# Performance work log

Measured on AMD Instinct MI355X. Metric: run time of the kernel, lower is better.

## Reference

```python
import jax, jax.numpy as jnp
import numpy as np

N_HEADS = 16


def setup_inputs() -> dict:
    key = jax.random.key(0)
    ks = jax.random.split(key, 5)
    E = 1024
    x = jax.random.normal(ks[0], (2, 2048, E), dtype=jnp.float32)
    s = 1.0 / np.sqrt(E)
    Wq = jax.random.normal(ks[1], (E, E), dtype=jnp.float32) * s
    Wk = jax.random.normal(ks[2], (E, E), dtype=jnp.float32) * s
    Wv = jax.random.normal(ks[3], (E, E), dtype=jnp.float32) * s
    Wo = jax.random.normal(ks[4], (E, E), dtype=jnp.float32) * s
    bo = jnp.zeros((E,), dtype=jnp.float32)
    return {"x": x, "Wq": Wq, "Wk": Wk, "Wv": Wv, "Wo": Wo, "bo": bo}


def reference(x, Wq, Wk, Wv, Wo, bo):
    B, S, E = x.shape
    H = N_HEADS
    D = E // H
    # project and split heads: [B, H, S, D]
    def split_heads(y):
        return y.reshape(B, S, H, D).transpose(0, 2, 1, 3)
    q = split_heads(x @ Wq)
    k = split_heads(x @ Wk)
    v = split_heads(x @ Wv)
    # full score matrix [B, H, S, S]
    scores = jnp.einsum('bhqd,bhkd->bhqk', q, k)
    causal = jnp.triu(jnp.ones((S, S), dtype=bool), k=1)
    scores = jnp.where(causal, -jnp.inf, scores)
    attn = jax.nn.softmax(scores / jnp.sqrt(jnp.float32(D)), axis=-1)
    # dropout rate is 0.0 -> identity
    ctx = jnp.einsum('bhqk,bhkd->bhqd', attn, v)
    ctx = ctx.transpose(0, 2, 1, 3).reshape(B, S, E)
    return ctx @ Wo + bo
```

## Files before the change

kernel.cpp:

```cpp
#include <hip/hip_runtime.h>
#include <stdint.h>


#define N_HEADS 16
#define HD 64
#define SEQ 2048
#define EMB 1024

typedef __attribute__((ext_vector_type(8))) short s16x8;
typedef __attribute__((ext_vector_type(4))) float f32x4;
typedef __attribute__((ext_vector_type(16))) float f32x16;

#define QSCALE 0.18033688f

template <bool B> struct BC { static constexpr bool value = B; };

__device__ __forceinline__ short f2b(float f) {
  union { float f; uint32_t u; } v; v.f = f;
  uint32_t u = v.u;
  u += 0x7fffu + ((u >> 16) & 1u);
  return (short)(u >> 16);
}

__device__ __forceinline__ uint32_t pk2(float a, float b) {
  union { float f; uint32_t u; } x, y; x.f = a; y.f = b;
  return ((x.u + 0x8000u) >> 16) | ((y.u + 0x8000u) & 0xffff0000u);
}

__device__ __forceinline__ float exp2a(float x) {
  float r; asm("v_exp_f32 %0, %1" : "=v"(r) : "v"(x)); return r;
}

__device__ __forceinline__ void gll16(const void* g, void* l) {
  __builtin_amdgcn_global_load_lds((const __attribute__((address_space(1))) void*)g,
                                   (__attribute__((address_space(3))) void*)l, 16, 0, 0);
}

#define SWZ(row, chunk) ((((row) * 8) + ((chunk) ^ ((row) & 7))) * 8)

__global__ __launch_bounds__(256) void k_prep(const float* __restrict__ x,
                                              const float* __restrict__ W0,
                                              const float* __restrict__ W1,
                                              const float* __restrict__ W2,
                                              const float* __restrict__ W3,
                                              short* __restrict__ xb,
                                              short* __restrict__ wt) {
  const int z = blockIdx.x, t = threadIdx.x;
  if (z < 4096) {
    int i = z * 256 + t;
    float4 v = ((const float4*)x)[i];
    short4 o;
    o.x = f2b(v.x); o.y = f2b(v.y); o.z = f2b(v.z); o.w = f2b(v.w);
    ((short4*)xb)[i] = o;
  } else {
    __shared__ float tile[32][33];
    int bz = z - 4096;
    int w = bz >> 10, rem = bz & 1023;
    int bn = (rem & 31) * 32, bk = (rem >> 5) * 32;
    const float* W = w == 0 ? W0 : w == 1 ? W1 : w == 2 ? W2 : W3;
    short* o = wt + (size_t)w * EMB * EMB;
    int tx = t & 31, ty = t >> 5;
    for (int i = ty; i < 32; i += 8)
      tile[i][tx] = W[(size_t)(bk + i) * EMB + bn + tx];
    __syncthreads();
    for (int i = ty; i < 32; i += 8)
      o[(size_t)(bn + i) * EMB + bk + tx] = f2b(tile[tx][i]);
  }
}

template <int MODE>
__global__ __launch_bounds__(256) void k_gemm(const short* __restrict__ A,
                                              const short* __restrict__ BT,
                                              void* __restrict__ outp,
                                              const float* __restrict__ bias) {
  constexpr int MAIN = 4 * 4096;
  constexpr int EPIL = (MODE == 1) ? 0 : 128 * 132;
  constexpr int SMSZ = MAIN > EPIL ? MAIN : EPIL;
  __shared__ alignas(16) short smem[SMSZ];

  const int t = threadIdx.x;
  const int by = blockIdx.y;
  const int m0 = blockIdx.x * 128;
  const short* Bp = BT + (size_t)by * (128 * EMB);
  const int wave = t >> 6, lane = t & 63;
  const int wm = (wave >> 1) * 64, wn = (wave & 1) * 64;
  const int l31 = lane & 31, lh = lane >> 5;

  const int srow = lane >> 2;
  const int soff = ((lane & 3) ^ (srow & 3)) * 8;

  auto stage = [&](int kb, int p) {
    short* as = smem + p * 4096;
    short* bs = smem + 8192 + p * 4096;
#pragma unroll
    for (int i = 0; i < 2; i++) {
      int rb = wave * 32 + i * 16;
      gll16(A + (size_t)(m0 + rb + srow) * EMB + kb + soff, &as[rb * 32]);
      gll16(Bp + (size_t)(rb + srow) * EMB + kb + soff, &bs[rb * 32]);
    }
  };
  auto frd = [&](const short* sb, int row, int kh) -> s16x8 {
    int c = kh * 2 + lh;
    return *(const s16x8*)&sb[row * 32 + ((c ^ (row & 3)) * 8)];
  };

  f32x16 acc[2][2] = {};

  auto kloop = [&](auto SWC) {
    constexpr bool SW = decltype(SWC)::value;
    int pb = 0;
    stage(0, 0);
    for (int kb = 0; kb < EMB; kb += 32) {
      __syncthreads();
      if (kb + 32 < EMB) stage(kb + 32, pb ^ 1);
      const short* as = smem + pb * 4096;
      const short* bs = smem + 8192 + pb * 4096;
      s16x8 af[2][2], bf[2][2];
#pragma unroll
      for (int mt = 0; mt < 2; mt++)
#pragma unroll
        for (int kh = 0; kh < 2; kh++) af[mt][kh] = frd(as, wm + mt * 32 + l31, kh);
#pragma unroll
      for (int nt = 0; nt < 2; nt++)
#pragma unroll
        for (int kh = 0; kh < 2; kh++) bf[nt][kh] = frd(bs, wn + nt * 32 + l31, kh);
#pragma unroll
      for (int mt = 0; mt < 2; mt++)
#pragma unroll
        for (int nt = 0; nt < 2; nt++)
#pragma unroll
          for (int kh = 0; kh < 2; kh++)
            acc[mt][nt] = SW
              ? __builtin_amdgcn_mfma_f32_32x32x16_bf16(bf[nt][kh], af[mt][kh], acc[mt][nt], 0, 0, 0)
              : __builtin_amdgcn_mfma_f32_32x32x16_bf16(af[mt][kh], bf[nt][kh], acc[mt][nt], 0, 0, 0);
      pb ^= 1;
    }
  };

  if (MODE == 1 || by < 16) kloop(BC<true>{});
  else                      kloop(BC<false>{});

  if (MODE == 0) {
    if (by < 16) {
      __syncthreads();
      short* Vls = smem;
      const int wsel = by >> 3;
      const float qs = (wsel == 0) ? QSCALE : 1.0f;
      const int n0l = (by & 7) * 128;
#pragma unroll
      for (int mt = 0; mt < 2; mt++) {
        int mr = wm + mt * 32 + l31;
#pragma unroll
        for (int nt = 0; nt < 2; nt++)
#pragma unroll
          for (int g = 0; g < 4; g++) {
            uint2 w;
            w.x = pk2(acc[mt][nt][4 * g + 0] * qs, acc[mt][nt][4 * g + 1] * qs);
            w.y = pk2(acc[mt][nt][4 * g + 2] * qs, acc[mt][nt][4 * g + 3] * qs);
            *(uint2*)&Vls[mr * 132 + wn + nt * 32 + g * 8 + 4 * lh] = w;
          }
      }
      __syncthreads();
      short* ob = (short*)outp + (size_t)wsel * (4u * 1024 * 1024);
      const int bb = m0 >> 11, ss0 = m0 & (SEQ - 1);
#pragma unroll
      for (int i = 0; i < 8; i++) {
        int mrow = i * 16 + (t >> 4);
        int ncol = (t & 15) * 8;
        int e = n0l + ncol, hh = e >> 6, dd = e & 63;
        *(uint4*)&ob[(((size_t)(bb * N_HEADS + hh) * SEQ) + ss0 + mrow) * 64 + dd] =
            *(const uint4*)&Vls[mrow * 132 + ncol];
      }
    } else {
      __syncthreads();
      short* Vls = smem;
#pragma unroll
      for (int nt = 0; nt < 2; nt++) {
        int nl = wn + nt * 32 + l31;
#pragma unroll
        for (int mt = 0; mt < 2; mt++)
#pragma unroll
          for (int g = 0; g < 4; g++) {
            uint2 w;
            w.x = pk2(acc[mt][nt][4 * g + 0], acc[mt][nt][4 * g + 1]);
            w.y = pk2(acc[mt][nt][4 * g + 2], acc[mt][nt][4 * g + 3]);
            *(uint2*)&Vls[nl * 132 + wm + mt * 32 + g * 8 + 4 * lh] = w;
          }
      }
      __syncthreads();
      short* obv = (short*)outp + (size_t)8 * 1024 * 1024;
      const int n0l = (by & 7) * 128;
      const int bb = m0 >> 11, ss0 = m0 & (SEQ - 1);
#pragma unroll
      for (int i = 0; i < 8; i++) {
        int nl = i * 16 + (t >> 4);
        int mc = (t & 15) * 8;
        int e = n0l + nl, hh = e >> 6, dd = e & 63;
        *(uint4*)&obv[((size_t)((bb * N_HEADS + hh) * HD + dd)) * SEQ + ss0 + mc] =
            *(const uint4*)&Vls[nl * 132 + mc];
      }
    }
  } else {
    float* of = (float*)outp;
    const int n0 = by * 128;
#pragma unroll
    for (int mt = 0; mt < 2; mt++) {
      int mg = m0 + wm + mt * 32 + l31;
#pragma unroll
      for (int nt = 0; nt < 2; nt++)
#pragma unroll
        for (int g = 0; g < 4; g++) {
          int ng = n0 + wn + nt * 32 + g * 8 + 4 * lh;
          f32x4 bv = *(const f32x4*)&bias[ng];
          f32x4 w;
          w[0] = acc[mt][nt][4 * g + 0] + bv[0];
          w[1] = acc[mt][nt][4 * g + 1] + bv[1];
          w[2] = acc[mt][nt][4 * g + 2] + bv[2];
          w[3] = acc[mt][nt][4 * g + 3] + bv[3];
          *(f32x4*)&of[(size_t)mg * EMB + ng] = w;
        }
    }
  }
}

__global__ __launch_bounds__(512) void k_attn(const short* __restrict__ Q,
                                              const short* __restrict__ K,
                                              const short* __restrict__ Vt,
                                              short* __restrict__ ctx) {
  __shared__ alignas(16) short UQP[128 * 72];
  __shared__ alignas(16) short Ks0[64 * 64], Ks1[64 * 64];
  __shared__ alignas(16) short Vs0[64 * 64], Vs1[64 * 64];

  const int t = threadIdx.x, wave = t >> 6, lane = t & 63;
  const int ml = lane & 15, quad = lane >> 4;
  const int bh = blockIdx.x;
  const int qb = 15 - (int)blockIdx.y;
  const size_t base = (size_t)bh * SEQ * HD;
  const int q0 = qb * 128, wq = q0 + wave * 16;

  const int sr = lane >> 3;
  const int sc = ((lane & 7) ^ sr) * 8;

#pragma unroll
  for (int i = 0; i < 2; i++) {
    int r8 = wave * 16 + i * 8;
    gll16(Q + base + (size_t)(q0 + r8 + sr) * HD + sc, &UQP[r8 * 64]);
  }
  auto stageKV = [&](int kt, short* kd, short* vd) {
    const int kbase = kt * 64;
    const int r8 = wave * 8;
    gll16(K + base + (size_t)(kbase + r8 + sr) * HD + sc, &kd[r8 * 64]);
    gll16(Vt + base + (size_t)(r8 + sr) * SEQ + kbase + sc, &vd[r8 * 64]);
  };

  f32x4 cacc[4] = {};
  float li = 0.f;
  short* Pw = &UQP[wave * 16 * 72];

  stageKV(0, Ks0, Vs0);
  __syncthreads();

  s16x8 qf[2];
#pragma unroll
  for (int c = 0; c < 2; c++)
    qf[c] = *(const s16x8*)&UQP[SWZ(wave * 16 + ml, 4 * c + quad)];
  __syncthreads();

  auto tile_body = [&](int kt, const short* kd, const short* vd) {
    const int kbase = kt * 64;
    if (kbase > wq + 15) return;
    const bool diag = (kbase + 63 > wq);
    f32x4 st[4];
#pragma unroll
    for (int nt = 0; nt < 4; nt++) {
      int row = nt * 16 + ml;
      s16x8 kf0 = *(const s16x8*)&kd[SWZ(row, quad)];
      s16x8 kf1 = *(const s16x8*)&kd[SWZ(row, 4 + quad)];
      f32x4 z = {};
      z = __builtin_amdgcn_mfma_f32_16x16x32_bf16(kf0, qf[0], z, 0, 0, 0);
      st[nt] = __builtin_amdgcn_mfma_f32_16x16x32_bf16(kf1, qf[1], z, 0, 0, 0);
    }
    const int qg = wq + ml;
    float rsum = 0.f;
#pragma unroll
    for (int nt = 0; nt < 4; nt++) {
      float p0 = exp2a(st[nt][0]);
      float p1 = exp2a(st[nt][1]);
      float p2 = exp2a(st[nt][2]);
      float p3 = exp2a(st[nt][3]);
      if (diag) {
        int kk = kbase + nt * 16 + quad * 4;
        if (kk + 0 > qg) p0 = 0.f;
        if (kk + 1 > qg) p1 = 0.f;
        if (kk + 2 > qg) p2 = 0.f;
        if (kk + 3 > qg) p3 = 0.f;
      }
      rsum += (p0 + p1) + (p2 + p3);
      uint2 w; w.x = pk2(p0, p1); w.y = pk2(p2, p3);
      *(uint2*)&Pw[ml * 72 + nt * 16 + quad * 4] = w;
    }
    li += rsum;
    __builtin_amdgcn_wave_barrier();

    s16x8 pf[2];
#pragma unroll
    for (int c = 0; c < 2; c++)
      pf[c] = *(const s16x8*)&Pw[ml * 72 + c * 32 + quad * 8];
#pragma unroll
    for (int mt = 0; mt < 4; mt++) {
      int row = mt * 16 + ml;
      s16x8 vf0 = *(const s16x8*)&vd[SWZ(row, quad)];
      s16x8 vf1 = *(const s16x8*)&vd[SWZ(row, 4 + quad)];
      cacc[mt] = __builtin_amdgcn_mfma_f32_16x16x32_bf16(vf0, pf[0], cacc[mt], 0, 0, 0);
      cacc[mt] = __builtin_amdgcn_mfma_f32_16x16x32_bf16(vf1, pf[1], cacc[mt], 0, 0, 0);
    }
  };

  const int nkt = 2 * qb + 2;
  for (int kt = 0; kt < nkt; kt += 2) {
    stageKV(kt + 1, Ks1, Vs1);
    tile_body(kt, Ks0, Vs0);
    __syncthreads();
    if (kt + 2 < nkt) stageKV(kt + 2, Ks0, Vs0);
    tile_body(kt + 1, Ks1, Vs1);
    __syncthreads();
  }

  li += __shfl_xor(li, 16, 64);
  li += __shfl_xor(li, 32, 64);
  float inv = 1.0f / li;
#pragma unroll
  for (int mt = 0; mt < 4; mt++) {
    uint2 w;
    w.x = pk2(cacc[mt][0] * inv, cacc[mt][1] * inv);
    w.y = pk2(cacc[mt][2] * inv, cacc[mt][3] * inv);
    *(uint2*)&Pw[ml * 72 + mt * 16 + quad * 4] = w;
  }
  __builtin_amdgcn_wave_barrier();
  const int b = bh >> 4, h = bh & 15;
#pragma unroll
  for (int i = 0; i < 2; i++) {
    int row = i * 8 + (lane >> 3);
    int q = wq + row;
    size_t gbase = ((size_t)(b * SEQ + q)) * EMB + h * 64 + (lane & 7) * 8;
    *(uint4*)&ctx[gbase] = *(const uint4*)&Pw[row * 72 + (lane & 7) * 8];
  }
}

extern "C" void kernel_launch(void* const* d_in, const int* in_sizes, int n_in,
                              void* d_out, int out_size, void* d_ws, size_t ws_size,
                              hipStream_t stream) {
  const float* x  = (const float*)d_in[0];
  const float* Wq = (const float*)d_in[1];
  const float* Wk = (const float*)d_in[2];
  const float* Wv = (const float*)d_in[3];
  const float* Wo = (const float*)d_in[4];
  const float* bo = (const float*)d_in[5];
  float* out = (float*)d_out;

  short* ws = (short*)d_ws;
  short* xb  = ws;
  short* wt  = ws + (size_t)4 * 1024 * 1024;
  short* qkv = ws + (size_t)8 * 1024 * 1024;

  k_prep<<<8192, 256, 0, stream>>>(x, Wq, Wk, Wv, Wo, xb, wt);
  k_gemm<0><<<dim3(32, 24), 256, 0, stream>>>(xb, wt, qkv, nullptr);
  k_attn<<<dim3(32, 16), 512, 0, stream>>>(qkv, qkv + (size_t)4 * 1024 * 1024,
                                           qkv + (size_t)8 * 1024 * 1024, xb);
  k_gemm<1><<<dim3(32, 8), 256, 0, stream>>>(xb, wt + (size_t)3 * 1024 * 1024, out, bo);
}
```

Before: 172.3 us.

## Add dedicated 256x256-tile QKV GEMM kernel with 4-stage async LDS pipeline

Replaces the 128x128-tile QKV projection GEMM with a new 512-thread kernel using 256x256 tiles and 16x16x32 bf16 MFMAs. It adds a 4-buffer global-to-LDS load pipeline with explicit vmcnt waits and raised wave priority around the MFMA bursts. The epilogue writes through LDS in two halves for the head-split Q/K and transposed V layouts, and k_gemm is reduced to the output-projection path only. The aim is more operand reuse per loaded byte and better overlap of loads with math. The trade-off is a grid of only 192 blocks, fewer than the CU count, and 128KB of LDS per block.

```diff
diff --git a/kernel.cpp b/kernel.cpp
--- a/kernel.cpp
+++ b/kernel.cpp
@@ -68,15 +68,149 @@
   }
 }
 
+__global__ __launch_bounds__(512, 2) void k_qkv(const short* __restrict__ A,
+                                                const short* __restrict__ BT,
+                                                short* __restrict__ qkv) {
+  __shared__ alignas(16) short smem[65536];
+  const int t = threadIdx.x;
+  const int bx = blockIdx.x, by = blockIdx.y;
+  const int m0 = bx * 256;
+  const short* Bp = BT + (size_t)by * (256 * EMB);
+  const int wave = t >> 6, lane = t & 63;
+  const int ml = lane & 15, quad = lane >> 4;
+  const int wm = (wave >> 2) * 128, wn = (wave & 3) * 64;
+  const int wsel = by >> 2;
+
+  auto stage = [&](int kt) {
+    short* sa = smem + (kt & 3) * 16384;
+    short* sb = sa + 8192;
+    const int k0 = kt * 32;
+#pragma unroll
+    for (int j = 0; j < 2; j++) {
+      int ci = j * 512 + t;
+      int r = ci >> 2;
+      int col = ((ci & 3) ^ (r & 3)) * 8;
+      size_t ldso = (size_t)(j * 512 + (t & ~63)) * 8;
+      gll16(A + (size_t)(m0 + r) * EMB + k0 + col, sa + ldso);
+      gll16(Bp + (size_t)r * EMB + k0 + col, sb + ldso);
+    }
+  };
+
+  f32x4 acc[8][4] = {};
+
+  stage(0); stage(1); stage(2);
+
+  auto kloop = [&](auto SWC) {
+    constexpr bool SW = decltype(SWC)::value;
+    for (int T = 0; T < 32; T++) {
+      const short* sa = smem + (T & 3) * 16384;
+      const short* sb = sa + 8192;
+      if (T < 30) asm volatile("s_waitcnt vmcnt(8)" ::: "memory");
+      else        asm volatile("s_waitcnt vmcnt(0)" ::: "memory");
+      __builtin_amdgcn_s_barrier();
+      __builtin_amdgcn_sched_barrier(0);
+      if (T + 3 < 32) stage(T + 3);
+      s16x8 af[8];
+#pragma unroll
+      for (int mt = 0; mt < 8; mt++) {
+        int row = wm + mt * 16 + ml;
+        af[mt] = *(const s16x8*)&sa[row * 32 + ((quad ^ (row & 3)) * 8)];
+      }
+#pragma unroll
+      for (int n2 = 0; n2 < 2; n2++) {
+        int r0 = wn + (n2 * 2 + 0) * 16 + ml;
+        int r1 = wn + (n2 * 2 + 1) * 16 + ml;
+        s16x8 b0 = *(const s16x8*)&sb[r0 * 32 + ((quad ^ (r0 & 3)) * 8)];
+        s16x8 b1 = *(const s16x8*)&sb[r1 * 32 + ((quad ^ (r1 & 3)) * 8)];
+        __builtin_amdgcn_s_setprio(1);
+#pragma unroll
+        for (int mt = 0; mt < 8; mt++) {
+          if (SW) {
+            acc[mt][n2 * 2 + 0] = __builtin_amdgcn_mfma_f32_16x16x32_bf16(b0, af[mt], acc[mt][n2 * 2 + 0], 0, 0, 0);
+            acc[mt][n2 * 2 + 1] = __builtin_amdgcn_mfma_f32_16x16x32_bf16(b1, af[mt], acc[mt][n2 * 2 + 1], 0, 0, 0);
+          } else {
+            acc[mt][n2 * 2 + 0] = __builtin_amdgcn_mfma_f32_16x16x32_bf16(af[mt], b0, acc[mt][n2 * 2 + 0], 0, 0, 0);
+            acc[mt][n2 * 2 + 1] = __builtin_amdgcn_mfma_f32_16x16x32_bf16(af[mt], b1, acc[mt][n2 * 2 + 1], 0, 0, 0);
+          }
+        }
+        __builtin_amdgcn_s_setprio(0);
+      }
+    }
+  };
+
+  if (wsel < 2) kloop(BC<true>{});
+  else          kloop(BC<false>{});
+
+  __syncthreads();
+
+  const int b = m0 >> 11, s0 = m0 & (SEQ - 1);
+  const int n0in = (by & 3) * 256;
+  if (wsel < 2) {
+    short* ob = qkv + (size_t)wsel * (4u * 1024 * 1024);
+    const float qs = (wsel == 0) ? QSCALE : 1.0f;
+#pragma unroll
+    for (int half = 0; half < 2; half++) {
+      if ((wm >> 7) == half) {
+#pragma unroll
+        for (int mt = 0; mt < 8; mt++) {
+          int lr = mt * 16 + ml;
+#pragma unroll
+          for (int nt = 0; nt < 4; nt++) {
+            uint2 w;
+            w.x = pk2(acc[mt][nt][0] * qs, acc[mt][nt][1] * qs);
+            w.y = pk2(acc[mt][nt][2] * qs, acc[mt][nt][3] * qs);
+            *(uint2*)&smem[lr * 264 + wn + nt * 16 + quad * 4] = w;
+          }
+        }
+      }
+      __syncthreads();
+#pragma unroll
+      for (int p = 0; p < 8; p++) {
+        int r = p * 16 + (t >> 5), c = t & 31;
+        int e = n0in + c * 8, hh = e >> 6, dd = e & 63;
+        *(uint4*)&ob[(((size_t)(b * N_HEADS + hh) * SEQ) + s0 + half * 128 + r) * 64 + dd] =
+            *(const uint4*)&smem[r * 264 + c * 8];
+      }
+      __syncthreads();
+    }
+  } else {
+    short* obv = qkv + (size_t)8 * 1024 * 1024;
+#pragma unroll
+    for (int half = 0; half < 2; half++) {
+      if ((wm >> 7) == half) {
+#pragma unroll
+        for (int mt = 0; mt < 8; mt++) {
+          int lr = mt * 16 + quad * 4;
+#pragma unroll
+          for (int nt = 0; nt < 4; nt++) {
+            int colL = wn + nt * 16 + ml;
+            uint2 w;
+            w.x = pk2(acc[mt][nt][0], acc[mt][nt][1]);
+            w.y = pk2(acc[mt][nt][2], acc[mt][nt][3]);
+            *(uint2*)&smem[colL * 136 + lr] = w;
+          }
+        }
+      }
+      __syncthreads();
+#pragma unroll
+      for (int p = 0; p < 8; p++) {
+        int colL = p * 32 + (t >> 4);
+        int sc = (t & 15) * 8;
+        int e = n0in + colL, hh = e >> 6, dd = e & 63;
+        *(uint4*)&obv[((size_t)(b * N_HEADS + hh) * HD + dd) * SEQ + s0 + half * 128 + sc] =
+            *(const uint4*)&smem[colL * 136 + sc];
+      }
+      __syncthreads();
+    }
+  }
+}
+
 template <int MODE>
 __global__ __launch_bounds__(256) void k_gemm(const short* __restrict__ A,
                                               const short* __restrict__ BT,
                                               void* __restrict__ outp,
                                               const float* __restrict__ bias) {
-  constexpr int MAIN = 4 * 4096;
-  constexpr int EPIL = (MODE == 1) ? 0 : 128 * 132;
-  constexpr int SMSZ = MAIN > EPIL ? MAIN : EPIL;
-  __shared__ alignas(16) short smem[SMSZ];
+  __shared__ alignas(16) short smem[4 * 4096];
 
   const int t = threadIdx.x;
   const int by = blockIdx.y;
@@ -106,8 +240,7 @@
 
   f32x16 acc[2][2] = {};
 
-  auto kloop = [&](auto SWC) {
-    constexpr bool SW = decltype(SWC)::value;
+  {
     int pb = 0;
     stage(0, 0);
     for (int kb = 0; kb < EMB; kb += 32) {
@@ -130,77 +263,12 @@
         for (int nt = 0; nt < 2; nt++)
 #pragma unroll
           for (int kh = 0; kh < 2; kh++)
-            acc[mt][nt] = SW
-              ? __builtin_amdgcn_mfma_f32_32x32x16_bf16(bf[nt][kh], af[mt][kh], acc[mt][nt], 0, 0, 0)
-              : __builtin_amdgcn_mfma_f32_32x32x16_bf16(af[mt][kh], bf[nt][kh], acc[mt][nt], 0, 0, 0);
+            acc[mt][nt] = __builtin_amdgcn_mfma_f32_32x32x16_bf16(bf[nt][kh], af[mt][kh], acc[mt][nt], 0, 0, 0);
       pb ^= 1;
     }
-  };
-
-  if (MODE == 1 || by < 16) kloop(BC<true>{});
-  else                      kloop(BC<false>{});
-
-  if (MODE == 0) {
-    if (by < 16) {
-      __syncthreads();
-      short* Vls = smem;
-      const int wsel = by >> 3;
-      const float qs = (wsel == 0) ? QSCALE : 1.0f;
-      const int n0l = (by & 7) * 128;
-#pragma unroll
-      for (int mt = 0; mt < 2; mt++) {
-        int mr = wm + mt * 32 + l31;
-#pragma unroll
-        for (int nt = 0; nt < 2; nt++)
-#pragma unroll
-          for (int g = 0; g < 4; g++) {
-            uint2 w;
-            w.x = pk2(acc[mt][nt][4 * g + 0] * qs, acc[mt][nt][4 * g + 1] * qs);
-            w.y = pk2(acc[mt][nt][4 * g + 2] * qs, acc[mt][nt][4 * g + 3] * qs);
-            *(uint2*)&Vls[mr * 132 + wn + nt * 32 + g * 8 + 4 * lh] = w;
-          }
-      }
-      __syncthreads();
-      short* ob = (short*)outp + (size_t)wsel * (4u * 1024 * 1024);
-      const int bb = m0 >> 11, ss0 = m0 & (SEQ - 1);
-#pragma unroll
-      for (int i = 0; i < 8; i++) {
-        int mrow = i * 16 + (t >> 4);
-        int ncol = (t & 15) * 8;
-        int e = n0l + ncol, hh = e >> 6, dd = e & 63;
-        *(uint4*)&ob[(((size_t)(bb * N_HEADS + hh) * SEQ) + ss0 + mrow) * 64 + dd] =
-            *(const uint4*)&Vls[mrow * 132 + ncol];
-      }
-    } else {
-      __syncthreads();
-      short* Vls = smem;
-#pragma unroll
-      for (int nt = 0; nt < 2; nt++) {
-        int nl = wn + nt * 32 + l31;
-#pragma unroll
-        for (int mt = 0; mt < 2; mt++)
-#pragma unroll
-          for (int g = 0; g < 4; g++) {
-            uint2 w;
-            w.x = pk2(acc[mt][nt][4 * g + 0], acc[mt][nt][4 * g + 1]);
-            w.y = pk2(acc[mt][nt][4 * g + 2], acc[mt][nt][4 * g + 3]);
-            *(uint2*)&Vls[nl * 132 + wm + mt * 32 + g * 8 + 4 * lh] = w;
-          }
-      }
-      __syncthreads();
-      short* obv = (short*)outp + (size_t)8 * 1024 * 1024;
-      const int n0l = (by & 7) * 128;
-      const int bb = m0 >> 11, ss0 = m0 & (SEQ - 1);
-#pragma unroll
-      for (int i = 0; i < 8; i++) {
-        int nl = i * 16 + (t >> 4);
-        int mc = (t & 15) * 8;
-        int e = n0l + nl, hh = e >> 6, dd = e & 63;
-        *(uint4*)&obv[((size_t)((bb * N_HEADS + hh) * HD + dd)) * SEQ + ss0 + mc] =
-            *(const uint4*)&Vls[nl * 132 + mc];
-      }
-    }
-  } else {
+  }
+
+  {
     float* of = (float*)outp;
     const int n0 = by * 128;
 #pragma unroll
@@ -364,7 +432,7 @@
   short* qkv = ws + (size_t)8 * 1024 * 1024;
 
   k_prep<<<8192, 256, 0, stream>>>(x, Wq, Wk, Wv, Wo, xb, wt);
-  k_gemm<0><<<dim3(32, 24), 256, 0, stream>>>(xb, wt, qkv, nullptr);
+  k_qkv<<<dim3(16, 12), 512, 0, stream>>>(xb, wt, qkv);
   k_attn<<<dim3(32, 16), 512, 0, stream>>>(qkv, qkv + (size_t)4 * 1024 * 1024,
                                            qkv + (size_t)8 * 1024 * 1024, xb);
   k_gemm<1><<<dim3(32, 8), 256, 0, stream>>>(xb, wt + (size_t)3 * 1024 * 1024, out, bo);
```

Result: no change. 174.1 us, median of 3 (+1.0%).
